# Kernel optimization log

Measured on AMD Instinct MI355X. Metric: run time of the kernel, lower is better.

Reference implementation:

```python
import jax, jax.numpy as jnp
import numpy as np

N, L, D, H, MLP_MULT = 2, 384, 512, 8, 4
HD = D // H
DM = D * MLP_MULT
EPS = 1e-5


def _linear_params(key, out_dim, in_dim, scale=0.02):
    kw, kb = jax.random.split(key)
    w = jax.random.normal(kw, (out_dim, in_dim), jnp.float32) * scale
    b = jax.random.normal(kb, (out_dim,), jnp.float32) * scale
    return w, b


def setup_inputs() -> dict:
    key = jax.random.key(0)
    ks = jax.random.split(key, 12)
    x = jax.random.normal(ks[0], (N, L, D), jnp.float32)
    mem = jax.random.normal(ks[1], (N, L, D), jnp.float32)
    pairwise_distances = jax.random.normal(ks[2], (N, L, L, D), jnp.float32)
    mem_padding_mask = jax.random.randint(ks[3], (N, L), 0, 2).astype(bool)
    qw, qb = _linear_params(ks[4], D, D)
    kvw, kvb = _linear_params(ks[5], 2 * D, D)
    pw, pb = _linear_params(ks[6], D, D)
    edw, edb = _linear_params(ks[7], H, D)
    w1, b1 = _linear_params(ks[8], DM, D)
    w2, b2 = _linear_params(ks[9], DM, DM)
    w3, b3 = _linear_params(ks[10], D, DM)
    return {
        'x': x, 'mem': mem, 'pairwise_distances': pairwise_distances,
        'mem_padding_mask': mem_padding_mask,
        'qw': qw, 'qb': qb, 'kvw': kvw, 'kvb': kvb, 'pw': pw, 'pb': pb,
        'edw': edw, 'edb': edb,
        'ln1_g': jnp.ones((D,), jnp.float32), 'ln1_b': jnp.zeros((D,), jnp.float32),
        'ln2_g': jnp.ones((D,), jnp.float32), 'ln2_b': jnp.zeros((D,), jnp.float32),
        'w1': w1, 'b1': b1, 'w2': w2, 'b2': b2, 'w3': w3, 'b3': b3,
    }


def _layernorm(x, g, b):
    m = jnp.mean(x, axis=-1, keepdims=True)
    v = jnp.mean((x - m) ** 2, axis=-1, keepdims=True)
    return (x - m) * jax.lax.rsqrt(v + EPS) * g + b


def reference(x, mem, pairwise_distances, mem_padding_mask,
              qw, qb, kvw, kvb, pw, pb, edw, edb,
              ln1_g, ln1_b, ln2_g, ln2_b,
              w1, b1, w2, b2, w3, b3):
    scale = HD ** -0.5
    a_in = _layernorm(x, ln1_g, ln1_b)
    a_mem = _layernorm(mem, ln1_g, ln1_b)

    q = (a_in @ qw.T + qb).reshape(N, L, H, HD).transpose(0, 2, 1, 3)   # (N,H,L1,HD)
    kv = (a_mem @ kvw.T + kvb).reshape(N, L, 2, H, HD)
    k = kv[:, :, 0].transpose(0, 2, 1, 3)                               # (N,H,L2,HD)
    v = kv[:, :, 1].transpose(0, 2, 1, 3)

    scores = jnp.einsum('bhid,bhjd->bhij', q, k) * scale                # (N,H,L1,L2)

    # T5-style relative position bias from pairwise distances
    bias = (pairwise_distances @ edw.T + edb)                            # (N,L1,L2,H)
    scores = scores + bias.transpose(0, 3, 1, 2)

    # padding mask (True = padded); rows that are fully padded get a zero
    # mask instead (then their output is zeroed after attention)
    all_pad = jnp.all(mem_padding_mask, axis=-1)                         # (N,)
    neg_inf = jnp.asarray(-jnp.inf, scores.dtype)
    mask = jnp.where(mem_padding_mask[:, None, None, :], neg_inf, 0.0)
    mask = jnp.where(all_pad[:, None, None, None], 0.0, mask)
    scores = scores + mask

    attn = jax.nn.softmax(scores, axis=-1)
    out = jnp.einsum('bhij,bhjd->bhid', attn, v)                         # (N,H,L1,HD)
    out = out * (~all_pad)[:, None, None, None]
    out = out.transpose(0, 2, 1, 3).reshape(N, L, D)

    x = x + (out @ pw.T + pb)

    h = _layernorm(x, ln2_g, ln2_b)
    h = jax.nn.silu(h @ w1.T + b1)
    h = jax.nn.silu(h @ w2.T + b2)
    h = h @ w3.T + b3
    return x + h
```

## Files before the change

kernel.cpp:

```cpp
#include <hip/hip_runtime.h>
#include <hip/hip_bf16.h>
#include <math.h>

#define NB   2
#define LSEQ 384
#define DMODEL 512
#define NH   8
#define HD2  64
#define DMLP 2048
#define LL2  (LSEQ*LSEQ)
#define ROWS (NB*LSEQ)

using bf16x8 = __attribute__((ext_vector_type(8))) short;
using f32x4  = __attribute__((ext_vector_type(4))) float;

__device__ __forceinline__ unsigned short f2bf(float f) {
    union { __hip_bfloat16 h; unsigned short u; } cv;
    cv.h = __float2bfloat16(f);
    return cv.u;
}

__device__ __forceinline__ void gload_lds16(const void* g, void* l) {
    __builtin_amdgcn_global_load_lds(
        (const __attribute__((address_space(1))) void*)g,
        (__attribute__((address_space(3))) void*)l, 16, 0, 0);
}

__global__ __launch_bounds__(256) void pre_kernel(
        const float* __restrict__ x, const float* __restrict__ mem,
        const float* __restrict__ ln1g, const float* __restrict__ ln1b,
        unsigned short* __restrict__ a_in, unsigned short* __restrict__ a_mem,
        const float* __restrict__ s0, const float* __restrict__ s1,
        const float* __restrict__ s2, const float* __restrict__ s3,
        const float* __restrict__ s4, const float* __restrict__ s5,
        const float* __restrict__ edw,
        unsigned short* __restrict__ d0, unsigned short* __restrict__ d1,
        unsigned short* __restrict__ d2, unsigned short* __restrict__ d3,
        unsigned short* __restrict__ d4, unsigned short* __restrict__ d5,
        unsigned short* __restrict__ edwb) {
    const int tid = threadIdx.x;
    if (blockIdx.x < 384) {
        int lane = tid & 63;
        int row  = blockIdx.x * 4 + (tid >> 6);
        const float* src = (row < ROWS) ? x : mem;
        unsigned short* dst = (row < ROWS) ? a_in : a_mem;
        int r2 = (row < ROWS) ? row : row - ROWS;
        const float* p = src + (size_t)r2 * DMODEL + lane * 8;
        float4 v0 = *(const float4*)p;
        float4 v1 = *(const float4*)(p + 4);
        float s  = v0.x + v0.y + v0.z + v0.w + v1.x + v1.y + v1.z + v1.w;
        float ss = v0.x*v0.x + v0.y*v0.y + v0.z*v0.z + v0.w*v0.w
                 + v1.x*v1.x + v1.y*v1.y + v1.z*v1.z + v1.w*v1.w;
        #pragma unroll
        for (int o = 32; o; o >>= 1) { s += __shfl_xor(s, o); ss += __shfl_xor(ss, o); }
        float m   = s * (1.0f / DMODEL);
        float var = ss * (1.0f / DMODEL) - m * m;
        float r   = rsqrtf(var + 1e-5f);
        float4 g0 = *(const float4*)(ln1g + lane * 8);
        float4 g1 = *(const float4*)(ln1g + lane * 8 + 4);
        float4 b0 = *(const float4*)(ln1b + lane * 8);
        float4 b1 = *(const float4*)(ln1b + lane * 8 + 4);
        unsigned short* q = dst + (size_t)r2 * DMODEL + lane * 8;
        ushort4 lo = {f2bf((v0.x-m)*r*g0.x+b0.x), f2bf((v0.y-m)*r*g0.y+b0.y),
                      f2bf((v0.z-m)*r*g0.z+b0.z), f2bf((v0.w-m)*r*g0.w+b0.w)};
        ushort4 hi = {f2bf((v1.x-m)*r*g1.x+b1.x), f2bf((v1.y-m)*r*g1.y+b1.y),
                      f2bf((v1.z-m)*r*g1.z+b1.z), f2bf((v1.w-m)*r*g1.w+b1.w)};
        *(ushort4*)q = lo;
        *(ushort4*)(q + 4) = hi;
        return;
    }
    const int stride = (gridDim.x - 384) * 256;
    const int t0 = (blockIdx.x - 384) * 256 + tid;
    const float* srcs[6] = {s0, s1, s2, s3, s4, s5};
    unsigned short* dsts[6] = {d0, d1, d2, d3, d4, d5};
    const int nf4[6] = {DMODEL*DMODEL/4, 2*DMODEL*DMODEL/4, DMODEL*DMODEL/4,
                        DMLP*DMODEL/4, DMLP*DMLP/4, DMLP*DMODEL/4};
    #pragma unroll
    for (int a = 0; a < 6; a++) {
        const float* s = srcs[a];
        unsigned short* d = dsts[a];
        for (int i = t0; i < nf4[a]; i += stride) {
            float4 v = *(const float4*)(s + (size_t)i * 4);
            ushort4 o = {f2bf(v.x), f2bf(v.y), f2bf(v.z), f2bf(v.w)};
            *(ushort4*)(d + (size_t)i * 4) = o;
        }
    }
    for (int i = t0; i < 16 * 512 / 4; i += stride) {
        int row = i >> 7;
        float4 v = {0.f, 0.f, 0.f, 0.f};
        if (row < 8) v = *(const float4*)(edw + (size_t)i * 4);
        ushort4 o = {f2bf(v.x), f2bf(v.y), f2bf(v.z), f2bf(v.w)};
        *(ushort4*)(edwb + (size_t)i * 4) = o;
    }
}

__global__ __launch_bounds__(256) void ln_kernel(const float* __restrict__ src0,
                                                 const float* __restrict__ g,
                                                 const float* __restrict__ b,
                                                 unsigned short* __restrict__ dst0) {
    int lane = threadIdx.x & 63;
    int row  = blockIdx.x * 4 + (threadIdx.x >> 6);
    const float* p = src0 + (size_t)row * DMODEL + lane * 8;
    float4 v0 = *(const float4*)p;
    float4 v1 = *(const float4*)(p + 4);
    float s  = v0.x + v0.y + v0.z + v0.w + v1.x + v1.y + v1.z + v1.w;
    float ss = v0.x*v0.x + v0.y*v0.y + v0.z*v0.z + v0.w*v0.w
             + v1.x*v1.x + v1.y*v1.y + v1.z*v1.z + v1.w*v1.w;
    #pragma unroll
    for (int o = 32; o; o >>= 1) { s += __shfl_xor(s, o); ss += __shfl_xor(ss, o); }
    float m   = s * (1.0f / DMODEL);
    float var = ss * (1.0f / DMODEL) - m * m;
    float r   = rsqrtf(var + 1e-5f);
    float4 g0 = *(const float4*)(g + lane * 8);
    float4 g1 = *(const float4*)(g + lane * 8 + 4);
    float4 b0 = *(const float4*)(b + lane * 8);
    float4 b1 = *(const float4*)(b + lane * 8 + 4);
    unsigned short* q = dst0 + (size_t)row * DMODEL + lane * 8;
    ushort4 lo = {f2bf((v0.x-m)*r*g0.x+b0.x), f2bf((v0.y-m)*r*g0.y+b0.y),
                  f2bf((v0.z-m)*r*g0.z+b0.z), f2bf((v0.w-m)*r*g0.w+b0.w)};
    ushort4 hi = {f2bf((v1.x-m)*r*g1.x+b1.x), f2bf((v1.y-m)*r*g1.y+b1.y),
                  f2bf((v1.z-m)*r*g1.z+b1.z), f2bf((v1.w-m)*r*g1.w+b1.w)};
    *(ushort4*)q = lo;
    *(ushort4*)(q + 4) = hi;
}

__global__ __launch_bounds__(256) void bias_mfma(const float* __restrict__ pd,
                                                 const unsigned short* __restrict__ edwb,
                                                 const float* __restrict__ edb,
                                                 const int* __restrict__ mask,
                                                 float* __restrict__ biasb) {
    __shared__ float Asb[3][64 * 64];
    const int tid = threadIdx.x;
    const int lane = tid & 63, w = tid >> 6;
    const int T = blockIdx.x;
    const size_t row0 = (size_t)T * 64;
    const int n = T / 2304;
    const int rem64 = (T - n * 2304) * 64;
    const int i = rem64 / LSEQ, j0 = rem64 % LSEQ;

    const int c = lane & 15, g = lane >> 4;
    bf16x8 bfv[8][2];
    #pragma unroll
    for (int kc = 0; kc < 8; kc++)
        #pragma unroll
        for (int ks = 0; ks < 2; ks++)
            bfv[kc][ks] = *(const bf16x8*)&edwb[c * 512 + kc * 64 + ks * 32 + g * 8];

    int pad = 1;
    for (int j = lane; j < LSEQ; j += 64) pad &= (mask[n * LSEQ + j] != 0) ? 1 : 0;
    unsigned long long bal = __ballot(pad);
    const int ap = (bal == ~0ull) ? 1 : 0;

    int rr[4], sc[4];
    #pragma unroll
    for (int q = 0; q < 4; q++) {
        int s = q * 256 + tid;
        rr[q] = s >> 4;
        int cs = s & 15;
        sc[q] = (cs & 8) | ((cs & 7) ^ (rr[q] & 7));
    }

    f32x4 acc = {};

    #pragma unroll
    for (int q = 0; q < 4; q++)
        gload_lds16(pd + (row0 + rr[q]) * DMODEL + sc[q] * 4, &Asb[0][(q * 256 + tid) * 4]);
    #pragma unroll
    for (int q = 0; q < 4; q++)
        gload_lds16(pd + (row0 + rr[q]) * DMODEL + 64 + sc[q] * 4, &Asb[1][(q * 256 + tid) * 4]);

    #pragma unroll
    for (int kc = 0; kc < 8; kc++) {
        if (kc < 7) asm volatile("s_waitcnt vmcnt(4)" ::: "memory");
        else        asm volatile("s_waitcnt vmcnt(0)" ::: "memory");
        __builtin_amdgcn_s_barrier();
        __builtin_amdgcn_sched_barrier(0);
        if (kc + 2 < 8) {
            const int nb = (kc + 2) % 3;
            #pragma unroll
            for (int q = 0; q < 4; q++)
                gload_lds16(pd + (row0 + rr[q]) * DMODEL + (kc + 2) * 64 + sc[q] * 4,
                            &Asb[nb][(q * 256 + tid) * 4]);
        }
        const float* Ab = &Asb[kc % 3][0];
        #pragma unroll
        for (int ks = 0; ks < 2; ks++) {
            const int ch0 = (8 * ks) | ((2 * g) ^ (c & 7));
            const int ch1 = (8 * ks) | ((2 * g + 1) ^ (c & 7));
            float4 a0 = *(const float4*)&Ab[(w * 16 + c) * 64 + ch0 * 4];
            float4 a1 = *(const float4*)&Ab[(w * 16 + c) * 64 + ch1 * 4];
            bf16x8 af;
            af[0] = (short)f2bf(a0.x); af[1] = (short)f2bf(a0.y);
            af[2] = (short)f2bf(a0.z); af[3] = (short)f2bf(a0.w);
            af[4] = (short)f2bf(a1.x); af[5] = (short)f2bf(a1.y);
            af[6] = (short)f2bf(a1.z); af[7] = (short)f2bf(a1.w);
            acc = __builtin_amdgcn_mfma_f32_16x16x32_bf16(af, bfv[kc][ks], acc, 0, 0, 0);
        }
    }

    if (c < 8) {
        const float eb = edb[c];
        const int jj = j0 + w * 16 + g * 4;
        int4 mv = *(const int4*)&mask[n * LSEQ + jj];
        const float NEGINF = -__builtin_inff();
        float4 o;
        o.x = acc[0] + eb + ((!ap && mv.x) ? NEGINF : 0.0f);
        o.y = acc[1] + eb + ((!ap && mv.y) ? NEGINF : 0.0f);
        o.z = acc[2] + eb + ((!ap && mv.z) ? NEGINF : 0.0f);
        o.w = acc[3] + eb + ((!ap && mv.w) ? NEGINF : 0.0f);
        *(float4*)&biasb[(size_t)(n * 8 + c) * LL2 + (size_t)i * LSEQ + jj] = o;
    }
}

template<int ACT, int RES, int OBF>
__device__ __forceinline__ void gemm_body(const unsigned short* __restrict__ A,
        const unsigned short* __restrict__ W, const float* __restrict__ bv,
        const float* __restrict__ Rsd, void* __restrict__ Cv,
        int Nn, int K, int m0, int n0, short* As, short* Ws) {
    const int tid  = threadIdx.x;
    const int lane = tid & 63, w = tid >> 6;
    const int wr = w >> 1, wc = w & 1;
    const int s0 = tid, s1 = 256 + tid;
    const int r0 = s0 >> 3, c0 = ((s0 & 7) ^ (r0 & 7)) << 3;
    const int r1 = s1 >> 3, c1 = ((s1 & 7) ^ (r1 & 7)) << 3;
    const unsigned short* ag0 = A + (size_t)(m0 + r0) * K + c0;
    const unsigned short* ag1 = A + (size_t)(m0 + r1) * K + c1;
    const unsigned short* wg0 = W + (size_t)(n0 + r0) * K + c0;
    const unsigned short* wg1 = W + (size_t)(n0 + r1) * K + c1;

    f32x4 acc[2][2] = {};
    const int lc = lane & 15, lr = lane >> 4;
    const int KT = K >> 6;

    #pragma unroll
    for (int t = 0; t < 4; t++) {
        const int b = t * 4096, k0 = t << 6;
        gload_lds16(ag0 + k0, &As[b + s0 * 8]);
        gload_lds16(ag1 + k0, &As[b + s1 * 8]);
        gload_lds16(wg0 + k0, &Ws[b + s0 * 8]);
        gload_lds16(wg1 + k0, &Ws[b + s1 * 8]);
    }

    for (int t = 0; t < KT; t++) {
        int rem = KT - 1 - t; if (rem > 3) rem = 3;
        if (rem >= 3)      asm volatile("s_waitcnt vmcnt(12)" ::: "memory");
        else if (rem == 2) asm volatile("s_waitcnt vmcnt(8)"  ::: "memory");
        else if (rem == 1) asm volatile("s_waitcnt vmcnt(4)"  ::: "memory");
        else               asm volatile("s_waitcnt vmcnt(0)"  ::: "memory");
        __builtin_amdgcn_s_barrier();
        __builtin_amdgcn_sched_barrier(0);
        const int cur = (t & 3) * 4096;
        bf16x8 af[2][2], bfr[2][2];
        #pragma unroll
        for (int m = 0; m < 2; m++) {
            const int rra = wr * 32 + m * 16 + lc;
            #pragma unroll
            for (int kk = 0; kk < 2; kk++) {
                const int cc = (lr + kk * 4) ^ (rra & 7);
                af[m][kk] = *(const bf16x8*)&As[cur + rra * 64 + cc * 8];
            }
        }
        #pragma unroll
        for (int nn = 0; nn < 2; nn++) {
            const int rrb = wc * 32 + nn * 16 + lc;
            #pragma unroll
            for (int kk = 0; kk < 2; kk++) {
                const int cc = (lr + kk * 4) ^ (rrb & 7);
                bfr[nn][kk] = *(const bf16x8*)&Ws[cur + rrb * 64 + cc * 8];
            }
        }
        #pragma unroll
        for (int m = 0; m < 2; m++)
            #pragma unroll
            for (int nn = 0; nn < 2; nn++) {
                acc[m][nn] = __builtin_amdgcn_mfma_f32_16x16x32_bf16(af[m][0], bfr[nn][0], acc[m][nn], 0, 0, 0);
                acc[m][nn] = __builtin_amdgcn_mfma_f32_16x16x32_bf16(af[m][1], bfr[nn][1], acc[m][nn], 0, 0, 0);
            }
        if (t + 4 < KT) {
            __builtin_amdgcn_sched_barrier(0);
            __builtin_amdgcn_s_barrier();
            const int b = cur, k0 = (t + 4) << 6;
            gload_lds16(ag0 + k0, &As[b + s0 * 8]);
            gload_lds16(ag1 + k0, &As[b + s1 * 8]);
            gload_lds16(wg0 + k0, &Ws[b + s0 * 8]);
            gload_lds16(wg1 + k0, &Ws[b + s1 * 8]);
        }
    }

    #pragma unroll
    for (int nn = 0; nn < 2; nn++) {
        int gcol = n0 + wc * 32 + nn * 16 + lc;
        float bb = bv[gcol];
        #pragma unroll
        for (int m = 0; m < 2; m++) {
            #pragma unroll
            for (int r = 0; r < 4; r++) {
                int grow = m0 + wr * 32 + m * 16 + lr * 4 + r;
                float o = acc[m][nn][r] + bb;
                if (ACT) o = o / (1.0f + expf(-o));
                if (RES) o += Rsd[(size_t)grow * Nn + gcol];
                if (OBF) ((unsigned short*)Cv)[(size_t)grow * Nn + gcol] = f2bf(o);
                else     ((float*)Cv)[(size_t)grow * Nn + gcol] = o;
            }
        }
    }
}

template<int ACT, int RES, int OBF>
__global__ __launch_bounds__(256) void mfma_gemm(const unsigned short* __restrict__ A,
                                                 const unsigned short* __restrict__ W,
                                                 const float* __restrict__ bv,
                                                 const float* __restrict__ Rsd,
                                                 void* __restrict__ Cv, int Nn, int K) {
    __shared__ short As[4 * 4096];
    __shared__ short Ws[4 * 4096];
    gemm_body<ACT, RES, OBF>(A, W, bv, Rsd, Cv, Nn, K, blockIdx.y * 64, blockIdx.x * 64, As, Ws);
}

__global__ __launch_bounds__(256) void qkv_gemm(const unsigned short* __restrict__ a_in,
                                                const unsigned short* __restrict__ a_mem,
                                                const unsigned short* __restrict__ qwb,
                                                const unsigned short* __restrict__ kvwb,
                                                const float* __restrict__ qbv,
                                                const float* __restrict__ kvbv,
                                                float* __restrict__ qbuf,
                                                float* __restrict__ kvbuf) {
    __shared__ short As[4 * 4096];
    __shared__ short Ws[4 * 4096];
    const int bx = blockIdx.x;
    const unsigned short* A; const unsigned short* W; const float* bv; float* C; int Nn, n0;
    if (bx < 8) { A = a_in;  W = qwb;  bv = qbv;  C = qbuf;  Nn = DMODEL;     n0 = bx * 64; }
    else        { A = a_mem; W = kvwb; bv = kvbv; C = kvbuf; Nn = 2 * DMODEL; n0 = (bx - 8) * 64; }
    gemm_body<0, 0, 0>(A, W, bv, nullptr, C, Nn, DMODEL, blockIdx.y * 64, n0, As, Ws);
}

__global__ __launch_bounds__(256) void scores_kernel(const float* __restrict__ q,
                                                     const float* __restrict__ kv,
                                                     const float* __restrict__ biasb,
                                                     float* __restrict__ S) {
    const int n = blockIdx.z, h = blockIdx.y;
    const int it = blockIdx.x / 12, jt = blockIdx.x % 12;
    __shared__ float Qs[64][32];
    __shared__ float Ks[64][32];
    const int tid = threadIdx.x;
    const int r = tid >> 3, c = (tid & 7) << 3;
    {
        const float* qp = q + ((size_t)(n * LSEQ + it * 32 + r)) * DMODEL + h * HD2 + c;
        float4 q0 = *(const float4*)qp;
        float4 q1 = *(const float4*)(qp + 4);
        Qs[c+0][r]=q0.x; Qs[c+1][r]=q0.y; Qs[c+2][r]=q0.z; Qs[c+3][r]=q0.w;
        Qs[c+4][r]=q1.x; Qs[c+5][r]=q1.y; Qs[c+6][r]=q1.z; Qs[c+7][r]=q1.w;
        const float* kp = kv + ((size_t)(n * LSEQ + jt * 32 + r)) * (2 * DMODEL) + h * HD2 + c;
        float4 k0 = *(const float4*)kp;
        float4 k1 = *(const float4*)(kp + 4);
        Ks[c+0][r]=k0.x; Ks[c+1][r]=k0.y; Ks[c+2][r]=k0.z; Ks[c+3][r]=k0.w;
        Ks[c+4][r]=k1.x; Ks[c+5][r]=k1.y; Ks[c+6][r]=k1.z; Ks[c+7][r]=k1.w;
    }
    __syncthreads();
    const int tx = tid & 15, ty = tid >> 4;
    float acc[2][2] = {{0.f,0.f},{0.f,0.f}};
    #pragma unroll
    for (int k = 0; k < 64; k++) {
        float2 a  = *(const float2*)&Qs[k][ty << 1];
        float2 b2 = *(const float2*)&Ks[k][tx << 1];
        acc[0][0] = fmaf(a.x, b2.x, acc[0][0]);
        acc[0][1] = fmaf(a.x, b2.y, acc[0][1]);
        acc[1][0] = fmaf(a.y, b2.x, acc[1][0]);
        acc[1][1] = fmaf(a.y, b2.y, acc[1][1]);
    }
    #pragma unroll
    for (int i2 = 0; i2 < 2; i2++) {
        int gi = it * 32 + (ty << 1) + i2;
        #pragma unroll
        for (int j2 = 0; j2 < 2; j2++) {
            int gj = jt * 32 + (tx << 1) + j2;
            size_t idx = ((size_t)(n * 8 + h)) * LL2 + (size_t)gi * LSEQ + gj;
            S[idx] = acc[i2][j2] * 0.125f + biasb[idx];
        }
    }
}

__global__ __launch_bounds__(256) void softmax_kernel(float* __restrict__ S) {
    int lane = threadIdx.x & 63;
    int row  = blockIdx.x * 4 + (threadIdx.x >> 6);
    float* p = S + (size_t)row * LSEQ;
    float v[6];
    #pragma unroll
    for (int cc = 0; cc < 6; cc++) v[cc] = p[cc * 64 + lane];
    float mx = v[0];
    #pragma unroll
    for (int cc = 1; cc < 6; cc++) mx = fmaxf(mx, v[cc]);
    #pragma unroll
    for (int o = 32; o; o >>= 1) mx = fmaxf(mx, __shfl_xor(mx, o));
    float sum = 0.f;
    #pragma unroll
    for (int cc = 0; cc < 6; cc++) { v[cc] = __expf(v[cc] - mx); sum += v[cc]; }
    #pragma unroll
    for (int o = 32; o; o >>= 1) sum += __shfl_xor(sum, o);
    float inv = 1.0f / sum;
    #pragma unroll
    for (int cc = 0; cc < 6; cc++) p[cc * 64 + lane] = v[cc] * inv;
}

__global__ __launch_bounds__(256) void av_kernel(const float* __restrict__ S,
                                                 const float* __restrict__ kv,
                                                 const int* __restrict__ mask,
                                                 unsigned short* __restrict__ outb) {
    const int it = blockIdx.x, h = blockIdx.y, n = blockIdx.z;
    __shared__ float Ps[32][68];
    __shared__ float Vs[64][68];
    const int tid = threadIdx.x;
    const int lane = tid & 63;
    int pad = 1;
    for (int j = lane; j < LSEQ; j += 64) pad &= (mask[n * LSEQ + j] != 0) ? 1 : 0;
    unsigned long long bal = __ballot(pad != 0);
    const float zf = (bal == 0xFFFFFFFFFFFFFFFFull) ? 0.0f : 1.0f;
    const int tx = tid & 15, ty = tid >> 4;
    const int pr = tid >> 3, pc = (tid & 7) << 3;
    const int vr = tid >> 2, vc = (tid & 3) << 4;
    float acc0[4] = {0,0,0,0}, acc1[4] = {0,0,0,0};
    for (int j0 = 0; j0 < LSEQ; j0 += 64) {
        const float* sp = S + ((size_t)(n * 8 + h)) * LL2 + (size_t)(it * 32 + pr) * LSEQ + j0 + pc;
        float4 p0 = *(const float4*)sp;
        float4 p1 = *(const float4*)(sp + 4);
        *(float4*)&Ps[pr][pc]     = p0;
        *(float4*)&Ps[pr][pc + 4] = p1;
        #pragma unroll
        for (int u = 0; u < 4; u++) {
            float4 vvv = *(const float4*)&kv[((size_t)(n * LSEQ + j0 + vr)) * (2 * DMODEL)
                                             + DMODEL + h * HD2 + vc + 4 * u];
            *(float4*)&Vs[vr][vc + 4 * u] = vvv;
        }
        __syncthreads();
        #pragma unroll
        for (int j = 0; j < 64; j++) {
            float pa  = Ps[ty][j];
            float pb2 = Ps[ty + 16][j];
            float4 vv = *(const float4*)&Vs[j][tx << 2];
            acc0[0] = fmaf(pa,  vv.x, acc0[0]);
            acc0[1] = fmaf(pa,  vv.y, acc0[1]);
            acc0[2] = fmaf(pa,  vv.z, acc0[2]);
            acc0[3] = fmaf(pa,  vv.w, acc0[3]);
            acc1[0] = fmaf(pb2, vv.x, acc1[0]);
            acc1[1] = fmaf(pb2, vv.y, acc1[1]);
            acc1[2] = fmaf(pb2, vv.z, acc1[2]);
            acc1[3] = fmaf(pb2, vv.w, acc1[3]);
        }
        __syncthreads();
    }
    int i0 = it * 32;
    ushort4 o0 = {f2bf(acc0[0]*zf), f2bf(acc0[1]*zf), f2bf(acc0[2]*zf), f2bf(acc0[3]*zf)};
    ushort4 o1 = {f2bf(acc1[0]*zf), f2bf(acc1[1]*zf), f2bf(acc1[2]*zf), f2bf(acc1[3]*zf)};
    *(ushort4*)&outb[((size_t)(n * LSEQ + i0 + ty)) * DMODEL + h * HD2 + (tx << 2)]      = o0;
    *(ushort4*)&outb[((size_t)(n * LSEQ + i0 + ty + 16)) * DMODEL + h * HD2 + (tx << 2)] = o1;
}

extern "C" void kernel_launch(void* const* d_in, const int* in_sizes, int n_in,
                              void* d_out, int out_size, void* d_ws, size_t ws_size,
                              hipStream_t stream) {
    const float* x    = (const float*)d_in[0];
    const float* mem  = (const float*)d_in[1];
    const float* pd   = (const float*)d_in[2];
    const int*   mask = (const int*)d_in[3];
    const float* qw   = (const float*)d_in[4];
    const float* qbv  = (const float*)d_in[5];
    const float* kvw  = (const float*)d_in[6];
    const float* kvbv = (const float*)d_in[7];
    const float* pw   = (const float*)d_in[8];
    const float* pbv  = (const float*)d_in[9];
    const float* edw  = (const float*)d_in[10];
    const float* edb  = (const float*)d_in[11];
    const float* ln1g = (const float*)d_in[12];
    const float* ln1b = (const float*)d_in[13];
    const float* ln2g = (const float*)d_in[14];
    const float* ln2b = (const float*)d_in[15];
    const float* w1   = (const float*)d_in[16];
    const float* b1   = (const float*)d_in[17];
    const float* w2   = (const float*)d_in[18];
    const float* b2   = (const float*)d_in[19];
    const float* w3   = (const float*)d_in[20];
    const float* b3   = (const float*)d_in[21];

    float* wsf = (float*)d_ws;
    float* biasb  = wsf + 16;
    float* scores = biasb + (size_t)NB * NH * LL2;
    float* qbuf   = scores + (size_t)NB * NH * LL2;
    float* kvbuf  = qbuf + (size_t)ROWS * DMODEL;
    float* x1buf  = kvbuf + (size_t)ROWS * 2 * DMODEL;
    unsigned short* a_in  = (unsigned short*)(x1buf + (size_t)ROWS * DMODEL);
    unsigned short* a_mem = a_in  + (size_t)ROWS * DMODEL;
    unsigned short* attno = a_mem + (size_t)ROWS * DMODEL;
    unsigned short* h0    = attno + (size_t)ROWS * DMODEL;
    unsigned short* h1    = h0    + (size_t)ROWS * DMODEL;
    unsigned short* h2    = h1    + (size_t)ROWS * DMLP;
    unsigned short* qwb   = h2    + (size_t)ROWS * DMLP;
    unsigned short* kvwb  = qwb   + (size_t)DMODEL * DMODEL;
    unsigned short* pwb   = kvwb  + (size_t)2 * DMODEL * DMODEL;
    unsigned short* w1b   = pwb   + (size_t)DMODEL * DMODEL;
    unsigned short* w2b   = w1b   + (size_t)DMLP * DMODEL;
    unsigned short* w3b   = w2b   + (size_t)DMLP * DMLP;
    unsigned short* edwb  = w3b   + (size_t)DMLP * DMODEL;

    float* outp = (float*)d_out;

    pre_kernel<<<2048, 256, 0, stream>>>(x, mem, ln1g, ln1b, a_in, a_mem,
                                         qw, kvw, pw, w1, w2, w3, edw,
                                         qwb, kvwb, pwb, w1b, w2b, w3b, edwb);
    bias_mfma<<<NB * LL2 / 64, 256, 0, stream>>>(pd, edwb, edb, mask, biasb);
    qkv_gemm<<<dim3(24, 12), 256, 0, stream>>>(a_in, a_mem, qwb, kvwb, qbv, kvbv, qbuf, kvbuf);

    scores_kernel<<<dim3(144, NH, NB), 256, 0, stream>>>(qbuf, kvbuf, biasb, scores);
    softmax_kernel<<<(NB * NH * LSEQ) / 4, 256, 0, stream>>>(scores);
    av_kernel<<<dim3(12, NH, NB), 256, 0, stream>>>(scores, kvbuf, mask, attno);

    mfma_gemm<0,1,0><<<dim3(8, 12), 256, 0, stream>>>(attno, pwb, pbv, x, x1buf, DMODEL, DMODEL);
    ln_kernel<<<ROWS / 4, 256, 0, stream>>>(x1buf, ln2g, ln2b, h0);
    mfma_gemm<1,0,1><<<dim3(32, 12), 256, 0, stream>>>(h0, w1b, b1, nullptr, h1, DMLP, DMODEL);
    mfma_gemm<1,0,1><<<dim3(32, 12), 256, 0, stream>>>(h1, w2b, b2, nullptr, h2, DMLP, DMLP);
    mfma_gemm<0,1,0><<<dim3(8, 12), 256, 0, stream>>>(h2, w3b, b3, x1buf, outp, DMODEL, DMLP);
}
```

Before: 272.5 us.

## Store attention bias in bf16 and simplify bias kernel pipeline to double buffering

The relative-position bias buffer moves from fp32 to bf16, which halves its write traffic in bias_mfma and its read traffic in scores_kernel. The bias kernel also drops from a three-stage LDS ring with manual vmcnt waits to a two-buffer scheme with __syncthreads, and now loads edw fragments inside the loop instead of keeping them in registers. The goal is to cut memory traffic and register pressure, but the simpler pipeline overlaps loads less and bf16 lowers the precision of the bias added to the scores.

```diff
diff --git a/kernel.cpp b/kernel.cpp
--- a/kernel.cpp
+++ b/kernel.cpp
@@ -18,6 +18,11 @@
     union { __hip_bfloat16 h; unsigned short u; } cv;
     cv.h = __float2bfloat16(f);
     return cv.u;
+}
+__device__ __forceinline__ float bf2f(unsigned short u) {
+    union { float f; unsigned int i; } c;
+    c.i = ((unsigned int)u) << 16;
+    return c.f;
 }
 
 __device__ __forceinline__ void gload_lds16(const void* g, void* l) {
@@ -128,8 +133,8 @@
                                                  const unsigned short* __restrict__ edwb,
                                                  const float* __restrict__ edb,
                                                  const int* __restrict__ mask,
-                                                 float* __restrict__ biasb) {
-    __shared__ float Asb[3][64 * 64];
+                                                 unsigned short* __restrict__ biasb) {
+    __shared__ float Asb[2][64 * 64];
     const int tid = threadIdx.x;
     const int lane = tid & 63, w = tid >> 6;
     const int T = blockIdx.x;
@@ -138,14 +143,6 @@
     const int rem64 = (T - n * 2304) * 64;
     const int i = rem64 / LSEQ, j0 = rem64 % LSEQ;
 
-    const int c = lane & 15, g = lane >> 4;
-    bf16x8 bfv[8][2];
-    #pragma unroll
-    for (int kc = 0; kc < 8; kc++)
-        #pragma unroll
-        for (int ks = 0; ks < 2; ks++)
-            bfv[kc][ks] = *(const bf16x8*)&edwb[c * 512 + kc * 64 + ks * 32 + g * 8];
-
     int pad = 1;
     for (int j = lane; j < LSEQ; j += 64) pad &= (mask[n * LSEQ + j] != 0) ? 1 : 0;
     unsigned long long bal = __ballot(pad);
@@ -160,29 +157,23 @@
         sc[q] = (cs & 8) | ((cs & 7) ^ (rr[q] & 7));
     }
 
+    const int c = lane & 15, g = lane >> 4;
     f32x4 acc = {};
 
     #pragma unroll
     for (int q = 0; q < 4; q++)
         gload_lds16(pd + (row0 + rr[q]) * DMODEL + sc[q] * 4, &Asb[0][(q * 256 + tid) * 4]);
-    #pragma unroll
-    for (int q = 0; q < 4; q++)
-        gload_lds16(pd + (row0 + rr[q]) * DMODEL + 64 + sc[q] * 4, &Asb[1][(q * 256 + tid) * 4]);
-
-    #pragma unroll
+    __syncthreads();
+
     for (int kc = 0; kc < 8; kc++) {
-        if (kc < 7) asm volatile("s_waitcnt vmcnt(4)" ::: "memory");
-        else        asm volatile("s_waitcnt vmcnt(0)" ::: "memory");
-        __builtin_amdgcn_s_barrier();
-        __builtin_amdgcn_sched_barrier(0);
-        if (kc + 2 < 8) {
-            const int nb = (kc + 2) % 3;
+        if (kc < 7) {
+            const int nb = (kc + 1) & 1;
             #pragma unroll
             for (int q = 0; q < 4; q++)
-                gload_lds16(pd + (row0 + rr[q]) * DMODEL + (kc + 2) * 64 + sc[q] * 4,
+                gload_lds16(pd + (row0 + rr[q]) * DMODEL + (kc + 1) * 64 + sc[q] * 4,
                             &Asb[nb][(q * 256 + tid) * 4]);
         }
-        const float* Ab = &Asb[kc % 3][0];
+        const float* Ab = &Asb[kc & 1][0];
         #pragma unroll
         for (int ks = 0; ks < 2; ks++) {
             const int ch0 = (8 * ks) | ((2 * g) ^ (c & 7));
@@ -194,8 +185,10 @@
             af[2] = (short)f2bf(a0.z); af[3] = (short)f2bf(a0.w);
             af[4] = (short)f2bf(a1.x); af[5] = (short)f2bf(a1.y);
             af[6] = (short)f2bf(a1.z); af[7] = (short)f2bf(a1.w);
-            acc = __builtin_amdgcn_mfma_f32_16x16x32_bf16(af, bfv[kc][ks], acc, 0, 0, 0);
-        }
+            bf16x8 bfv = *(const bf16x8*)&edwb[c * 512 + kc * 64 + ks * 32 + g * 8];
+            acc = __builtin_amdgcn_mfma_f32_16x16x32_bf16(af, bfv, acc, 0, 0, 0);
+        }
+        if (kc < 7) __syncthreads();
     }
 
     if (c < 8) {
@@ -203,12 +196,12 @@
         const int jj = j0 + w * 16 + g * 4;
         int4 mv = *(const int4*)&mask[n * LSEQ + jj];
         const float NEGINF = -__builtin_inff();
-        float4 o;
-        o.x = acc[0] + eb + ((!ap && mv.x) ? NEGINF : 0.0f);
-        o.y = acc[1] + eb + ((!ap && mv.y) ? NEGINF : 0.0f);
-        o.z = acc[2] + eb + ((!ap && mv.z) ? NEGINF : 0.0f);
-        o.w = acc[3] + eb + ((!ap && mv.w) ? NEGINF : 0.0f);
-        *(float4*)&biasb[(size_t)(n * 8 + c) * LL2 + (size_t)i * LSEQ + jj] = o;
+        ushort4 o;
+        o.x = f2bf(acc[0] + eb + ((!ap && mv.x) ? NEGINF : 0.0f));
+        o.y = f2bf(acc[1] + eb + ((!ap && mv.y) ? NEGINF : 0.0f));
+        o.z = f2bf(acc[2] + eb + ((!ap && mv.z) ? NEGINF : 0.0f));
+        o.w = f2bf(acc[3] + eb + ((!ap && mv.w) ? NEGINF : 0.0f));
+        *(ushort4*)&biasb[(size_t)(n * 8 + c) * LL2 + (size_t)i * LSEQ + jj] = o;
     }
 }
 
@@ -336,7 +329,7 @@
 
 __global__ __launch_bounds__(256) void scores_kernel(const float* __restrict__ q,
                                                      const float* __restrict__ kv,
-                                                     const float* __restrict__ biasb,
+                                                     const unsigned short* __restrict__ biasb,
                                                      float* __restrict__ S) {
     const int n = blockIdx.z, h = blockIdx.y;
     const int it = blockIdx.x / 12, jt = blockIdx.x % 12;
@@ -371,12 +364,11 @@
     #pragma unroll
     for (int i2 = 0; i2 < 2; i2++) {
         int gi = it * 32 + (ty << 1) + i2;
-        #pragma unroll
-        for (int j2 = 0; j2 < 2; j2++) {
-            int gj = jt * 32 + (tx << 1) + j2;
-            size_t idx = ((size_t)(n * 8 + h)) * LL2 + (size_t)gi * LSEQ + gj;
-            S[idx] = acc[i2][j2] * 0.125f + biasb[idx];
-        }
+        int gj = jt * 32 + (tx << 1);
+        size_t idx = ((size_t)(n * 8 + h)) * LL2 + (size_t)gi * LSEQ + gj;
+        ushort2 bb = *(const ushort2*)&biasb[idx];
+        S[idx]     = acc[i2][0] * 0.125f + bf2f(bb.x);
+        S[idx + 1] = acc[i2][1] * 0.125f + bf2f(bb.y);
     }
 }
 
@@ -482,8 +474,8 @@
     const float* b3   = (const float*)d_in[21];
 
     float* wsf = (float*)d_ws;
-    float* biasb  = wsf + 16;
-    float* scores = biasb + (size_t)NB * NH * LL2;
+    unsigned short* biasb = (unsigned short*)(wsf + 16);
+    float* scores = wsf + 16 + (size_t)NB * NH * LL2 / 2;
     float* qbuf   = scores + (size_t)NB * NH * LL2;
     float* kvbuf  = qbuf + (size_t)ROWS * DMODEL;
     float* x1buf  = kvbuf + (size_t)ROWS * 2 * DMODEL;
```

Measured after the change: 259.4 us. 1.05x faster.
